# Performance work log

Hardware: AMD Instinct MI355X
Metric: run time of the kernel (lower is better)

## Reference

```python
import jax, jax.numpy as jnp
import numpy as np
import math

N_HEADS = 16

def _rope_tables(T, D, dtype):
    # inv_freq over even dims, emb = [freqs, freqs] -> [T, D]
    inv_freq = 1.0 / (10000.0 ** (jnp.arange(0, D, 2, dtype=jnp.float32) / D))
    freqs = jnp.arange(T, dtype=jnp.float32)[:, None] * inv_freq[None, :]  # [T, D/2]
    emb = jnp.concatenate([freqs, freqs], axis=-1)  # [T, D]
    return jnp.cos(emb).astype(dtype), jnp.sin(emb).astype(dtype)

def _rotate_half(x):
    d = x.shape[-1] // 2
    return jnp.concatenate([-x[..., d:], x[..., :d]], axis=-1)

def setup_inputs() -> dict:
    key = jax.random.key(0)
    ks = jax.random.split(key, 5)
    B, T, C = 2, 2048, 1024
    s = 1.0 / math.sqrt(C)
    return {
        "x": jax.random.normal(ks[0], (B, T, C), dtype=jnp.float32),
        "Wq": jax.random.normal(ks[1], (C, C), dtype=jnp.float32) * s,
        "Wk": jax.random.normal(ks[2], (C, C), dtype=jnp.float32) * s,
        "Wv": jax.random.normal(ks[3], (C, C), dtype=jnp.float32) * s,
        "Wo": jax.random.normal(ks[4], (C, C), dtype=jnp.float32) * s,
    }

def reference(x, Wq, Wk, Wv, Wo):
    B, T, C = x.shape
    H = N_HEADS
    D = C // H
    # QKV projections (torch Linear, bias=False: y = x @ W.T), split into heads
    def proj(W):
        return (x @ W.T).reshape(B, T, H, D).transpose(0, 2, 1, 3)  # [B,H,T,D]
    q, k, v = proj(Wq), proj(Wk), proj(Wv)
    # RoPE
    cos, sin = _rope_tables(T, D, x.dtype)  # [T,D] each, broadcast over B,H
    q = q * cos + _rotate_half(q) * sin
    k = k * cos + _rotate_half(k) * sin
    # scaled dot-product attention with causal mask
    scale = 1.0 / math.sqrt(D)
    attn = jnp.einsum('bhtd,bhsd->bhts', q, k) * scale  # [B,H,T,T]
    row = jnp.arange(T)[:, None]
    col = jnp.arange(T)[None, :]
    attn = jnp.where(col > row, -jnp.inf, attn)
    p = jax.nn.softmax(attn, axis=-1)
    out = jnp.einsum('bhts,bhsd->bhtd', p, v)  # [B,H,T,D]
    out = out.transpose(0, 2, 1, 3).reshape(B, T, C)
    return out @ Wo.T
```

## Files before the change

### kernel.cpp

```cpp
#include <hip/hip_runtime.h>
#include <hip/hip_bf16.h>


typedef __hip_bfloat16 bf16;
typedef __attribute__((ext_vector_type(8))) short bf16x8;
typedef __attribute__((ext_vector_type(4))) float f32x4;
typedef __attribute__((ext_vector_type(4))) short short4v;

#define MFMA16(a, b, c) __builtin_amdgcn_mfma_f32_16x16x32_bf16((a), (b), (c), 0, 0, 0)

constexpr int Bn = 2, Hn = 16, Tn = 2048, Dn = 64, Cn = 1024;
constexpr size_t NE = (size_t)Bn * Tn * Cn;
constexpr size_t WE = (size_t)Cn * Cn;

__device__ inline unsigned short bfbits(float x) {
    bf16 b = __float2bfloat16(x);
    return *(unsigned short*)&b;
}

__device__ inline bf16x8 pack8(f32x4 a, f32x4 b) {
    bf16x8 r;
#pragma unroll
    for (int i = 0; i < 4; ++i) r[i] = (short)bfbits(a[i]);
#pragma unroll
    for (int i = 0; i < 4; ++i) r[4 + i] = (short)bfbits(b[i]);
    return r;
}

__device__ inline void gl_lds16(const bf16* g, unsigned short* l) {
    __builtin_amdgcn_global_load_lds(
        (const __attribute__((address_space(1))) void*)g,
        (__attribute__((address_space(3))) void*)l, 16, 0, 0);
}

__device__ inline void stage128(const bf16* gbase, int ld, unsigned short* lds,
                                int wave, int lane) {
#pragma unroll
    for (int j = 0; j < 4; ++j) {
        int p = j * 256 + wave * 64 + lane;
        int row = p >> 3, ch = (p & 7) ^ (row & 7);
        gl_lds16(gbase + (size_t)row * ld + ch * 8,
                 lds + (size_t)(j * 256 + wave * 64) * 8);
    }
}
__device__ inline void stage64(const bf16* gbase, int ld, unsigned short* lds,
                               int wave, int lane) {
#pragma unroll
    for (int j = 0; j < 2; ++j) {
        int p = j * 256 + wave * 64 + lane;
        int row = p >> 3, ch = (p & 7) ^ (row & 7);
        gl_lds16(gbase + (size_t)row * ld + ch * 8,
                 lds + (size_t)(j * 256 + wave * 64) * 8);
    }
}

__device__ inline bf16x8 ldsfrag(const unsigned short* base, int row, int ch) {
    return *(const bf16x8*)&base[row * 64 + ((ch ^ (row & 7)) * 8)];
}

__global__ __launch_bounds__(256) void convert_kernel(
    const float* __restrict__ x, const float* __restrict__ wq,
    const float* __restrict__ wk, const float* __restrict__ wv,
    const float* __restrict__ wo, bf16* __restrict__ dst)
{
    int blk = blockIdx.x;
    const float* src;
    size_t doff;
    if (blk < 2048) {
        src = x + (size_t)blk * 2048;
        doff = (size_t)blk * 2048;
    } else {
        int w = (blk - 2048) >> 9, b = (blk - 2048) & 511;
        const float* s4[4] = {wq, wk, wv, wo};
        src = s4[w] + (size_t)b * 2048;
        doff = NE + (size_t)w * WE + (size_t)b * 2048;
    }
    int t = threadIdx.x * 8;
    f32x4 a = *(const f32x4*)(src + t);
    f32x4 b2 = *(const f32x4*)(src + t + 4);
    *(bf16x8*)(dst + doff + t) = pack8(a, b2);
}

__global__ __launch_bounds__(256) void gemm_qkv_kernel(
    const bf16* __restrict__ X, const bf16* __restrict__ Wbase,
    bf16* __restrict__ Qo, bf16* __restrict__ Ko, bf16* __restrict__ Vo)
{
    __shared__ unsigned short As[128 * 64];
    __shared__ unsigned short Bs[128 * 64];
    const int bm = blockIdx.x, bn = blockIdx.y, wsel = blockIdx.z;
    const bf16* W = Wbase + (size_t)wsel * WE;
    const int tid  = threadIdx.x;
    const int wave = tid >> 6, lane = tid & 63;
    const int lx   = lane & 15, quad = lane >> 4;
    const int wm = wave >> 1, wn = wave & 1;

    const bf16* abase = X + (size_t)(bm * 128) * Cn;
    const bf16* bbase = W + (size_t)(bn * 128) * Cn;

    f32x4 acc[4][4] = {};
    for (int kt = 0; kt < Cn / 64; ++kt) {
        __syncthreads();
        stage128(abase + kt * 64, Cn, As, wave, lane);
        stage128(bbase + kt * 64, Cn, Bs, wave, lane);
        __syncthreads();
#pragma unroll
        for (int ks = 0; ks < 2; ++ks) {
            bf16x8 af[4], bfv[4];
#pragma unroll
            for (int mt = 0; mt < 4; ++mt)
                af[mt] = ldsfrag(As, wm * 64 + mt * 16 + lx, ks * 4 + quad);
#pragma unroll
            for (int nt = 0; nt < 4; ++nt)
                bfv[nt] = ldsfrag(Bs, wn * 64 + nt * 16 + lx, ks * 4 + quad);
#pragma unroll
            for (int mt = 0; mt < 4; ++mt)
#pragma unroll
                for (int nt = 0; nt < 4; ++nt)
                    acc[mt][nt] = MFMA16(af[mt], bfv[nt], acc[mt][nt]);
        }
    }

    const int h = bn * 2 + wn;
    if (wsel <= 1) {
#pragma unroll
        for (int mt = 0; mt < 4; ++mt)
#pragma unroll
            for (int r = 0; r < 4; ++r) {
                int mg = bm * 128 + wm * 64 + mt * 16 + quad * 4 + r;
                int t  = mg & (Tn - 1);
#pragma unroll
                for (int nt = 0; nt < 2; ++nt) {
                    int d = nt * 16 + lx;
                    float ang = (float)t * __expf(-(float)d * 0.2878231366f);
                    float c, s;
                    __sincosf(ang, &s, &c);
                    float a0 = acc[mt][nt][r], a1 = acc[mt][nt + 2][r];
                    acc[mt][nt][r]     = a0 * c - a1 * s;
                    acc[mt][nt + 2][r] = a1 * c + a0 * s;
                }
            }
    }

#pragma unroll
    for (int mt = 0; mt < 4; ++mt) {
        int mg0 = bm * 128 + wm * 64 + mt * 16 + quad * 4;
        int b = mg0 >> 11, t0 = mg0 & (Tn - 1);
        if (wsel == 0) {
#pragma unroll
            for (int nt = 0; nt < 4; ++nt)
#pragma unroll
                for (int r = 0; r < 4; ++r) {
                    int d = nt * 16 + lx;
                    Qo[((size_t)(b * Hn + h) * Tn + t0 + r) * Dn + d] =
                        __float2bfloat16(acc[mt][nt][r] * 0.125f);
                }
        } else if (wsel == 1) {
#pragma unroll
            for (int nt = 0; nt < 4; ++nt)
#pragma unroll
                for (int r = 0; r < 4; ++r) {
                    int d = nt * 16 + lx;
                    Ko[((size_t)(b * Hn + h) * Tn + t0 + r) * Dn + d] =
                        __float2bfloat16(acc[mt][nt][r]);
                }
        } else {
#pragma unroll
            for (int nt = 0; nt < 4; ++nt) {
                int d = nt * 16 + lx;
                short4v pk;
#pragma unroll
                for (int r = 0; r < 4; ++r) pk[r] = (short)bfbits(acc[mt][nt][r]);
                *(short4v*)&Vo[((size_t)(b * Hn + h) * Dn + d) * Tn + t0] = pk;
            }
        }
    }
}

__global__ __launch_bounds__(256) void gemm_out_kernel(
    const bf16* __restrict__ A, const bf16* __restrict__ W, float* __restrict__ Out)
{
    __shared__ unsigned short As[128 * 64];
    __shared__ unsigned short Bs[64 * 64];
    const int bm = blockIdx.x, bn = blockIdx.y;
    const int tid  = threadIdx.x;
    const int wave = tid >> 6, lane = tid & 63;
    const int lx   = lane & 15, quad = lane >> 4;
    const int wm = wave >> 1, wn = wave & 1;

    const bf16* abase = A + (size_t)(bm * 128) * Cn;
    const bf16* bbase = W + (size_t)(bn * 64) * Cn;

    f32x4 acc[4][2] = {};
    for (int kt = 0; kt < Cn / 64; ++kt) {
        __syncthreads();
        stage128(abase + kt * 64, Cn, As, wave, lane);
        stage64(bbase + kt * 64, Cn, Bs, wave, lane);
        __syncthreads();
#pragma unroll
        for (int ks = 0; ks < 2; ++ks) {
            bf16x8 af[4], bfv[2];
#pragma unroll
            for (int mt = 0; mt < 4; ++mt)
                af[mt] = ldsfrag(As, wm * 64 + mt * 16 + lx, ks * 4 + quad);
#pragma unroll
            for (int nt = 0; nt < 2; ++nt)
                bfv[nt] = ldsfrag(Bs, wn * 32 + nt * 16 + lx, ks * 4 + quad);
#pragma unroll
            for (int mt = 0; mt < 4; ++mt)
#pragma unroll
                for (int nt = 0; nt < 2; ++nt)
                    acc[mt][nt] = MFMA16(af[mt], bfv[nt], acc[mt][nt]);
        }
    }
#pragma unroll
    for (int mt = 0; mt < 4; ++mt)
#pragma unroll
        for (int nt = 0; nt < 2; ++nt)
#pragma unroll
            for (int r = 0; r < 4; ++r) {
                int mg = bm * 128 + wm * 64 + mt * 16 + quad * 4 + r;
                int ng = bn * 64 + wn * 32 + nt * 16 + lx;
                Out[(size_t)mg * Cn + ng] = acc[mt][nt][r];
            }
}

__global__ __launch_bounds__(256) void attn_kernel(
    const bf16* __restrict__ Q, const bf16* __restrict__ K,
    const bf16* __restrict__ Vt, bf16* __restrict__ O)
{
    __shared__ unsigned short Ks[64 * 64];
    __shared__ unsigned short Vs[64 * 64];
    __shared__ unsigned short Pl[4][16 * 72];
    const int f  = blockIdx.x;
    const int bh = (f & 7) * 4 + ((f >> 3) & 3);
    const int qb = 31 - (f >> 5);
    const int tid  = threadIdx.x;
    const int wave = tid >> 6, lane = tid & 63;
    const int lx   = lane & 15, quad = lane >> 4;

    const bf16* Qh = Q  + (size_t)bh * Tn * Dn;
    const bf16* Kh = K  + (size_t)bh * Tn * Dn;
    const bf16* Vh = Vt + (size_t)bh * Dn * Tn;
    unsigned short* pw = &Pl[wave][0];

    const int qrowA = qb * 64 + wave * 16 + lx;
    bf16x8 aq0 = *(const bf16x8*)(Qh + (size_t)qrowA * Dn + quad * 8);
    bf16x8 aq1 = *(const bf16x8*)(Qh + (size_t)qrowA * Dn + 32 + quad * 8);

    bf16x8 ones;
#pragma unroll
    for (int i = 0; i < 8; ++i) ones[i] = (short)0x3F80;

    f32x4 acc_o[4] = {};
    f32x4 acc_l = {};
    const int row_local = wave * 16 + quad * 4;

    for (int c = 0; c <= qb; ++c) {
        __syncthreads();
        stage64(Kh + (size_t)c * 64 * Dn, Dn, Ks, wave, lane);
        stage64(Vh + (size_t)c * 64, Tn, Vs, wave, lane);
        __syncthreads();
        f32x4 accs[4] = {};
#pragma unroll
        for (int nt = 0; nt < 4; ++nt) {
            int key = nt * 16 + lx;
            bf16x8 k0 = ldsfrag(Ks, key, quad);
            bf16x8 k1 = ldsfrag(Ks, key, quad + 4);
            accs[nt] = MFMA16(aq0, k0, accs[nt]);
            accs[nt] = MFMA16(aq1, k1, accs[nt]);
        }
        if (c < qb) {
#pragma unroll
            for (int nt = 0; nt < 4; ++nt)
#pragma unroll
                for (int r = 0; r < 4; ++r)
                    pw[(quad * 4 + r) * 72 + nt * 16 + lx] = bfbits(__expf(accs[nt][r]));
        } else {
#pragma unroll
            for (int nt = 0; nt < 4; ++nt) {
                int keyl = nt * 16 + lx;
#pragma unroll
                for (int r = 0; r < 4; ++r) {
                    float p = (keyl > row_local + r) ? 0.0f : __expf(accs[nt][r]);
                    pw[(quad * 4 + r) * 72 + nt * 16 + lx] = bfbits(p);
                }
            }
        }
        asm volatile("s_waitcnt lgkmcnt(0)" ::: "memory");
        bf16x8 ap0 = *(const bf16x8*)&pw[lx * 72 + quad * 8];
        bf16x8 ap1 = *(const bf16x8*)&pw[lx * 72 + 32 + quad * 8];
        acc_l = MFMA16(ap0, ones, acc_l);
        acc_l = MFMA16(ap1, ones, acc_l);
#pragma unroll
        for (int dt = 0; dt < 4; ++dt) {
            int d = dt * 16 + lx;
            bf16x8 v0 = ldsfrag(Vs, d, quad);
            bf16x8 v1 = ldsfrag(Vs, d, quad + 4);
            acc_o[dt] = MFMA16(ap0, v0, acc_o[dt]);
            acc_o[dt] = MFMA16(ap1, v1, acc_o[dt]);
        }
    }

    const int b = bh >> 4, h = bh & 15;
#pragma unroll
    for (int dt = 0; dt < 4; ++dt)
#pragma unroll
        for (int r = 0; r < 4; ++r) {
            int t = qb * 64 + row_local + r;
            int d = dt * 16 + lx;
            float o = acc_o[dt][r] / acc_l[r];
            O[((size_t)(b * Tn + t) * Hn + h) * Dn + d] = __float2bfloat16(o);
        }
}

extern "C" void kernel_launch(void* const* d_in, const int* in_sizes, int n_in,
                              void* d_out, int out_size, void* d_ws, size_t ws_size,
                              hipStream_t stream)
{
    const float* x  = (const float*)d_in[0];
    const float* Wq = (const float*)d_in[1];
    const float* Wk = (const float*)d_in[2];
    const float* Wv = (const float*)d_in[3];
    const float* Wo = (const float*)d_in[4];
    float* out = (float*)d_out;

    bf16* ws = (bf16*)d_ws;
    bf16* Xb = ws;
    bf16* Wb = ws + NE;
    bf16* Qb = ws + NE + 4 * WE;
    bf16* Kb = Qb + NE;
    bf16* Vb = Kb + NE;
    bf16* Ab = Xb;

    convert_kernel<<<4096, 256, 0, stream>>>(x, Wq, Wk, Wv, Wo, ws);
    gemm_qkv_kernel<<<dim3(32, 8, 3), 256, 0, stream>>>(Xb, Wb, Qb, Kb, Vb);
    attn_kernel<<<1024, 256, 0, stream>>>(Qb, Kb, Vb, Ab);
    gemm_out_kernel<<<dim3(32, 16), 256, 0, stream>>>(Ab, Wb + 3 * WE, out);
}
```

Before: 177.4 us.

## Load GEMM weight fragments directly from global and enlarge attention query tile

Both projection GEMMs stop staging the weight tile in shared memory. Each wave now loads its B fragments straight from global memory into registers, which removes LDS traffic and shrinks shared memory use, but the loads are issued per wave and may duplicate global reads across waves. The attention kernel now has each block handle 128 query rows (32 per wave) instead of 64, and the grid is halved. Each staged K/V chunk is therefore reused across twice as many rows, at the cost of more registers and fewer blocks.

Result: slower. 219.7 us (+23.8%).

```diff
diff --git a/kernel.cpp b/kernel.cpp
--- a/kernel.cpp
+++ b/kernel.cpp
@@ -86,7 +86,6 @@
     bf16* __restrict__ Qo, bf16* __restrict__ Ko, bf16* __restrict__ Vo)
 {
     __shared__ unsigned short As[128 * 64];
-    __shared__ unsigned short Bs[128 * 64];
     const int bm = blockIdx.x, bn = blockIdx.y, wsel = blockIdx.z;
     const bf16* W = Wbase + (size_t)wsel * WE;
     const int tid  = threadIdx.x;
@@ -95,28 +94,33 @@
     const int wm = wave >> 1, wn = wave & 1;
 
     const bf16* abase = X + (size_t)(bm * 128) * Cn;
-    const bf16* bbase = W + (size_t)(bn * 128) * Cn;
+    const bf16* wr[4];
+#pragma unroll
+    for (int nt = 0; nt < 4; ++nt)
+        wr[nt] = W + (size_t)(bn * 128 + wn * 64 + nt * 16 + lx) * Cn + quad * 8;
 
     f32x4 acc[4][4] = {};
     for (int kt = 0; kt < Cn / 64; ++kt) {
         __syncthreads();
         stage128(abase + kt * 64, Cn, As, wave, lane);
-        stage128(bbase + kt * 64, Cn, Bs, wave, lane);
+        bf16x8 bfv[4][2];
+#pragma unroll
+        for (int nt = 0; nt < 4; ++nt)
+#pragma unroll
+            for (int ks = 0; ks < 2; ++ks)
+                bfv[nt][ks] = *(const bf16x8*)(wr[nt] + kt * 64 + ks * 32);
         __syncthreads();
 #pragma unroll
         for (int ks = 0; ks < 2; ++ks) {
-            bf16x8 af[4], bfv[4];
+            bf16x8 af[4];
 #pragma unroll
             for (int mt = 0; mt < 4; ++mt)
                 af[mt] = ldsfrag(As, wm * 64 + mt * 16 + lx, ks * 4 + quad);
 #pragma unroll
-            for (int nt = 0; nt < 4; ++nt)
-                bfv[nt] = ldsfrag(Bs, wn * 64 + nt * 16 + lx, ks * 4 + quad);
-#pragma unroll
             for (int mt = 0; mt < 4; ++mt)
 #pragma unroll
                 for (int nt = 0; nt < 4; ++nt)
-                    acc[mt][nt] = MFMA16(af[mt], bfv[nt], acc[mt][nt]);
+                    acc[mt][nt] = MFMA16(af[mt], bfv[nt][ks], acc[mt][nt]);
         }
     }
 
@@ -180,7 +184,6 @@
     const bf16* __restrict__ A, const bf16* __restrict__ W, float* __restrict__ Out)
 {
     __shared__ unsigned short As[128 * 64];
-    __shared__ unsigned short Bs[64 * 64];
     const int bm = blockIdx.x, bn = blockIdx.y;
     const int tid  = threadIdx.x;
     const int wave = tid >> 6, lane = tid & 63;
@@ -188,28 +191,33 @@
     const int wm = wave >> 1, wn = wave & 1;
 
     const bf16* abase = A + (size_t)(bm * 128) * Cn;
-    const bf16* bbase = W + (size_t)(bn * 64) * Cn;
+    const bf16* wr[2];
+#pragma unroll
+    for (int nt = 0; nt < 2; ++nt)
+        wr[nt] = W + (size_t)(bn * 64 + wn * 32 + nt * 16 + lx) * Cn + quad * 8;
 
     f32x4 acc[4][2] = {};
     for (int kt = 0; kt < Cn / 64; ++kt) {
         __syncthreads();
         stage128(abase + kt * 64, Cn, As, wave, lane);
-        stage64(bbase + kt * 64, Cn, Bs, wave, lane);
+        bf16x8 bfv[2][2];
+#pragma unroll
+        for (int nt = 0; nt < 2; ++nt)
+#pragma unroll
+            for (int ks = 0; ks < 2; ++ks)
+                bfv[nt][ks] = *(const bf16x8*)(wr[nt] + kt * 64 + ks * 32);
         __syncthreads();
 #pragma unroll
         for (int ks = 0; ks < 2; ++ks) {
-            bf16x8 af[4], bfv[2];
+            bf16x8 af[4];
 #pragma unroll
             for (int mt = 0; mt < 4; ++mt)
                 af[mt] = ldsfrag(As, wm * 64 + mt * 16 + lx, ks * 4 + quad);
 #pragma unroll
-            for (int nt = 0; nt < 2; ++nt)
-                bfv[nt] = ldsfrag(Bs, wn * 32 + nt * 16 + lx, ks * 4 + quad);
-#pragma unroll
             for (int mt = 0; mt < 4; ++mt)
 #pragma unroll
                 for (int nt = 0; nt < 2; ++nt)
-                    acc[mt][nt] = MFMA16(af[mt], bfv[nt], acc[mt][nt]);
+                    acc[mt][nt] = MFMA16(af[mt], bfv[nt][ks], acc[mt][nt]);
         }
     }
 #pragma unroll
@@ -230,10 +238,10 @@
 {
     __shared__ unsigned short Ks[64 * 64];
     __shared__ unsigned short Vs[64 * 64];
-    __shared__ unsigned short Pl[4][16 * 72];
+    __shared__ unsigned short Pl[4][32 * 72];
     const int f  = blockIdx.x;
     const int bh = (f & 7) * 4 + ((f >> 3) & 3);
-    const int qb = 31 - (f >> 5);
+    const int qt = 15 - (f >> 5);
     const int tid  = threadIdx.x;
     const int wave = tid >> 6, lane = tid & 63;
     const int lx   = lane & 15, quad = lane >> 4;
@@ -243,74 +251,100 @@
     const bf16* Vh = Vt + (size_t)bh * Dn * Tn;
     unsigned short* pw = &Pl[wave][0];
 
-    const int qrowA = qb * 64 + wave * 16 + lx;
-    bf16x8 aq0 = *(const bf16x8*)(Qh + (size_t)qrowA * Dn + quad * 8);
-    bf16x8 aq1 = *(const bf16x8*)(Qh + (size_t)qrowA * Dn + 32 + quad * 8);
+    const int row0 = qt * 128 + wave * 32;
+    bf16x8 aq[2][2];
+#pragma unroll
+    for (int mt = 0; mt < 2; ++mt)
+#pragma unroll
+        for (int ks = 0; ks < 2; ++ks)
+            aq[mt][ks] = *(const bf16x8*)(Qh + (size_t)(row0 + mt * 16 + lx) * Dn
+                                          + ks * 32 + quad * 8);
 
     bf16x8 ones;
 #pragma unroll
     for (int i = 0; i < 8; ++i) ones[i] = (short)0x3F80;
 
-    f32x4 acc_o[4] = {};
-    f32x4 acc_l = {};
-    const int row_local = wave * 16 + quad * 4;
-
-    for (int c = 0; c <= qb; ++c) {
+    f32x4 acc_o[2][4] = {};
+    f32x4 acc_l[2] = {};
+    const int cmax = 2 * qt + 1;
+
+    for (int c = 0; c <= cmax; ++c) {
         __syncthreads();
         stage64(Kh + (size_t)c * 64 * Dn, Dn, Ks, wave, lane);
         stage64(Vh + (size_t)c * 64, Tn, Vs, wave, lane);
         __syncthreads();
-        f32x4 accs[4] = {};
+        f32x4 s[2][4] = {};
 #pragma unroll
         for (int nt = 0; nt < 4; ++nt) {
             int key = nt * 16 + lx;
             bf16x8 k0 = ldsfrag(Ks, key, quad);
             bf16x8 k1 = ldsfrag(Ks, key, quad + 4);
-            accs[nt] = MFMA16(aq0, k0, accs[nt]);
-            accs[nt] = MFMA16(aq1, k1, accs[nt]);
-        }
-        if (c < qb) {
-#pragma unroll
-            for (int nt = 0; nt < 4; ++nt)
-#pragma unroll
-                for (int r = 0; r < 4; ++r)
-                    pw[(quad * 4 + r) * 72 + nt * 16 + lx] = bfbits(__expf(accs[nt][r]));
+#pragma unroll
+            for (int mt = 0; mt < 2; ++mt) {
+                s[mt][nt] = MFMA16(aq[mt][0], k0, s[mt][nt]);
+                s[mt][nt] = MFMA16(aq[mt][1], k1, s[mt][nt]);
+            }
+        }
+        if (c < 2 * qt) {
+#pragma unroll
+            for (int mt = 0; mt < 2; ++mt)
+#pragma unroll
+                for (int nt = 0; nt < 4; ++nt)
+#pragma unroll
+                    for (int r = 0; r < 4; ++r)
+                        pw[(mt * 16 + quad * 4 + r) * 72 + nt * 16 + lx] =
+                            bfbits(__expf(s[mt][nt][r]));
         } else {
 #pragma unroll
-            for (int nt = 0; nt < 4; ++nt) {
-                int keyl = nt * 16 + lx;
-#pragma unroll
-                for (int r = 0; r < 4; ++r) {
-                    float p = (keyl > row_local + r) ? 0.0f : __expf(accs[nt][r]);
-                    pw[(quad * 4 + r) * 72 + nt * 16 + lx] = bfbits(p);
+            for (int mt = 0; mt < 2; ++mt)
+#pragma unroll
+                for (int nt = 0; nt < 4; ++nt) {
+                    int keyg = c * 64 + nt * 16 + lx;
+#pragma unroll
+                    for (int r = 0; r < 4; ++r) {
+                        int rowg = qt * 128 + wave * 32 + mt * 16 + quad * 4 + r;
+                        float p = (keyg > rowg) ? 0.0f : __expf(s[mt][nt][r]);
+                        pw[(mt * 16 + quad * 4 + r) * 72 + nt * 16 + lx] = bfbits(p);
+                    }
                 }
-            }
         }
         asm volatile("s_waitcnt lgkmcnt(0)" ::: "memory");
-        bf16x8 ap0 = *(const bf16x8*)&pw[lx * 72 + quad * 8];
-        bf16x8 ap1 = *(const bf16x8*)&pw[lx * 72 + 32 + quad * 8];
-        acc_l = MFMA16(ap0, ones, acc_l);
-        acc_l = MFMA16(ap1, ones, acc_l);
+        bf16x8 ap[2][2];
+#pragma unroll
+        for (int mt = 0; mt < 2; ++mt)
+#pragma unroll
+            for (int ks = 0; ks < 2; ++ks)
+                ap[mt][ks] = *(const bf16x8*)&pw[(mt * 16 + lx) * 72 + ks * 32 + quad * 8];
+#pragma unroll
+        for (int mt = 0; mt < 2; ++mt) {
+            acc_l[mt] = MFMA16(ap[mt][0], ones, acc_l[mt]);
+            acc_l[mt] = MFMA16(ap[mt][1], ones, acc_l[mt]);
+        }
 #pragma unroll
         for (int dt = 0; dt < 4; ++dt) {
             int d = dt * 16 + lx;
             bf16x8 v0 = ldsfrag(Vs, d, quad);
             bf16x8 v1 = ldsfrag(Vs, d, quad + 4);
-            acc_o[dt] = MFMA16(ap0, v0, acc_o[dt]);
-            acc_o[dt] = MFMA16(ap1, v1, acc_o[dt]);
+#pragma unroll
+            for (int mt = 0; mt < 2; ++mt) {
+                acc_o[mt][dt] = MFMA16(ap[mt][0], v0, acc_o[mt][dt]);
+                acc_o[mt][dt] = MFMA16(ap[mt][1], v1, acc_o[mt][dt]);
+            }
         }
     }
 
     const int b = bh >> 4, h = bh & 15;
 #pragma unroll
-    for (int dt = 0; dt < 4; ++dt)
-#pragma unroll
-        for (int r = 0; r < 4; ++r) {
-            int t = qb * 64 + row_local + r;
-            int d = dt * 16 + lx;
-            float o = acc_o[dt][r] / acc_l[r];
-            O[((size_t)(b * Tn + t) * Hn + h) * Dn + d] = __float2bfloat16(o);
-        }
+    for (int mt = 0; mt < 2; ++mt)
+#pragma unroll
+        for (int dt = 0; dt < 4; ++dt)
+#pragma unroll
+            for (int r = 0; r < 4; ++r) {
+                int t = row0 + mt * 16 + quad * 4 + r;
+                int d = dt * 16 + lx;
+                float o = acc_o[mt][dt][r] / acc_l[mt][r];
+                O[((size_t)(b * Tn + t) * Hn + h) * Dn + d] = __float2bfloat16(o);
+            }
 }
 
 extern "C" void kernel_launch(void* const* d_in, const int* in_sizes, int n_in,
@@ -334,6 +368,6 @@
 
     convert_kernel<<<4096, 256, 0, stream>>>(x, Wq, Wk, Wv, Wo, ws);
     gemm_qkv_kernel<<<dim3(32, 8, 3), 256, 0, stream>>>(Xb, Wb, Qb, Kb, Vb);
-    attn_kernel<<<1024, 256, 0, stream>>>(Qb, Kb, Vb, Ab);
+    attn_kernel<<<512, 256, 0, stream>>>(Qb, Kb, Vb, Ab);
     gemm_out_kernel<<<dim3(32, 16), 256, 0, stream>>>(Ab, Wb + 3 * WE, out);
 }
```

## Pre-swizzle weights into MFMA fragment layout and load B directly to registers

Applied to the files above, without the earlier changes.

The fp32-to-bf16 conversion kernel now writes each weight matrix in a fragment-major layout that matches the 16x16x32 MFMA B-operand. The QKV and output GEMMs then load B fragments straight from global memory into registers with coalesced 16-byte loads, skipping LDS staging for B. This removes half of the LDS traffic and shared memory, which may raise occupancy. The cost is that each wave loads its own B fragments from global/L2 with no sharing across waves through LDS, and the loads sit between the barriers, so latency may be exposed.

After: 178.5 us. Within noise of the previous version (+0.6%).

```diff
diff --git a/kernel.cpp b/kernel.cpp
--- a/kernel.cpp
+++ b/kernel.cpp
@@ -64,21 +64,26 @@
     const float* __restrict__ wo, bf16* __restrict__ dst)
 {
     int blk = blockIdx.x;
-    const float* src;
-    size_t doff;
     if (blk < 2048) {
-        src = x + (size_t)blk * 2048;
-        doff = (size_t)blk * 2048;
+        const float* src = x + (size_t)blk * 2048;
+        int t = threadIdx.x * 8;
+        f32x4 a = *(const f32x4*)(src + t);
+        f32x4 b2 = *(const f32x4*)(src + t + 4);
+        *(bf16x8*)(dst + (size_t)blk * 2048 + t) = pack8(a, b2);
     } else {
         int w = (blk - 2048) >> 9, b = (blk - 2048) & 511;
         const float* s4[4] = {wq, wk, wv, wo};
-        src = s4[w] + (size_t)b * 2048;
-        doff = NE + (size_t)w * WE + (size_t)b * 2048;
-    }
-    int t = threadIdx.x * 8;
-    f32x4 a = *(const f32x4*)(src + t);
-    f32x4 b2 = *(const f32x4*)(src + t + 4);
-    *(bf16x8*)(dst + doff + t) = pack8(a, b2);
+        const float* W = s4[w];
+        int frag = b * 4 + (threadIdx.x >> 6);
+        int lane = threadIdx.x & 63;
+        int lx = lane & 15, quad = lane >> 4;
+        int nb = frag >> 5, kc = frag & 31;
+        const float* src = W + (size_t)(nb * 16 + lx) * Cn + kc * 32 + quad * 8;
+        f32x4 a = *(const f32x4*)(src);
+        f32x4 b2 = *(const f32x4*)(src + 4);
+        *(bf16x8*)(dst + NE + (size_t)w * WE + (size_t)frag * 512 + lane * 8) =
+            pack8(a, b2);
+    }
 }
 
 __global__ __launch_bounds__(256) void gemm_qkv_kernel(
@@ -86,7 +91,6 @@
     bf16* __restrict__ Qo, bf16* __restrict__ Ko, bf16* __restrict__ Vo)
 {
     __shared__ unsigned short As[128 * 64];
-    __shared__ unsigned short Bs[128 * 64];
     const int bm = blockIdx.x, bn = blockIdx.y, wsel = blockIdx.z;
     const bf16* W = Wbase + (size_t)wsel * WE;
     const int tid  = threadIdx.x;
@@ -95,28 +99,32 @@
     const int wm = wave >> 1, wn = wave & 1;
 
     const bf16* abase = X + (size_t)(bm * 128) * Cn;
-    const bf16* bbase = W + (size_t)(bn * 128) * Cn;
+    const int nb0 = bn * 8 + wn * 4;
+    const bf16* wfrag = W + (size_t)nb0 * 32 * 512 + (size_t)lane * 8;
 
     f32x4 acc[4][4] = {};
     for (int kt = 0; kt < Cn / 64; ++kt) {
         __syncthreads();
         stage128(abase + kt * 64, Cn, As, wave, lane);
-        stage128(bbase + kt * 64, Cn, Bs, wave, lane);
+        bf16x8 bfv[4][2];
+#pragma unroll
+        for (int nt = 0; nt < 4; ++nt)
+#pragma unroll
+            for (int ks = 0; ks < 2; ++ks)
+                bfv[nt][ks] = *(const bf16x8*)(wfrag +
+                    ((size_t)nt * 32 + kt * 2 + ks) * 512);
         __syncthreads();
 #pragma unroll
         for (int ks = 0; ks < 2; ++ks) {
-            bf16x8 af[4], bfv[4];
+            bf16x8 af[4];
 #pragma unroll
             for (int mt = 0; mt < 4; ++mt)
                 af[mt] = ldsfrag(As, wm * 64 + mt * 16 + lx, ks * 4 + quad);
 #pragma unroll
-            for (int nt = 0; nt < 4; ++nt)
-                bfv[nt] = ldsfrag(Bs, wn * 64 + nt * 16 + lx, ks * 4 + quad);
-#pragma unroll
             for (int mt = 0; mt < 4; ++mt)
 #pragma unroll
                 for (int nt = 0; nt < 4; ++nt)
-                    acc[mt][nt] = MFMA16(af[mt], bfv[nt], acc[mt][nt]);
+                    acc[mt][nt] = MFMA16(af[mt], bfv[nt][ks], acc[mt][nt]);
         }
     }
 
@@ -180,7 +188,6 @@
     const bf16* __restrict__ A, const bf16* __restrict__ W, float* __restrict__ Out)
 {
     __shared__ unsigned short As[128 * 64];
-    __shared__ unsigned short Bs[64 * 64];
     const int bm = blockIdx.x, bn = blockIdx.y;
     const int tid  = threadIdx.x;
     const int wave = tid >> 6, lane = tid & 63;
@@ -188,28 +195,32 @@
     const int wm = wave >> 1, wn = wave & 1;
 
     const bf16* abase = A + (size_t)(bm * 128) * Cn;
-    const bf16* bbase = W + (size_t)(bn * 64) * Cn;
+    const int nb0 = bn * 4 + wn * 2;
+    const bf16* wfrag = W + (size_t)nb0 * 32 * 512 + (size_t)lane * 8;
 
     f32x4 acc[4][2] = {};
     for (int kt = 0; kt < Cn / 64; ++kt) {
         __syncthreads();
         stage128(abase + kt * 64, Cn, As, wave, lane);
-        stage64(bbase + kt * 64, Cn, Bs, wave, lane);
+        bf16x8 bfv[2][2];
+#pragma unroll
+        for (int nt = 0; nt < 2; ++nt)
+#pragma unroll
+            for (int ks = 0; ks < 2; ++ks)
+                bfv[nt][ks] = *(const bf16x8*)(wfrag +
+                    ((size_t)nt * 32 + kt * 2 + ks) * 512);
         __syncthreads();
 #pragma unroll
         for (int ks = 0; ks < 2; ++ks) {
-            bf16x8 af[4], bfv[2];
+            bf16x8 af[4];
 #pragma unroll
             for (int mt = 0; mt < 4; ++mt)
                 af[mt] = ldsfrag(As, wm * 64 + mt * 16 + lx, ks * 4 + quad);
 #pragma unroll
-            for (int nt = 0; nt < 2; ++nt)
-                bfv[nt] = ldsfrag(Bs, wn * 32 + nt * 16 + lx, ks * 4 + quad);
-#pragma unroll
             for (int mt = 0; mt < 4; ++mt)
 #pragma unroll
                 for (int nt = 0; nt < 2; ++nt)
-                    acc[mt][nt] = MFMA16(af[mt], bfv[nt], acc[mt][nt]);
+                    acc[mt][nt] = MFMA16(af[mt], bfv[nt][ks], acc[mt][nt]);
         }
     }
 #pragma unroll
```
